# Kernel optimization log

Hardware: AMD Instinct MI355X
Metric: run time of the kernel (lower is better)

Reference implementation:

```python
import jax, jax.numpy as jnp
import numpy as np

DIM = 1024
N_HEADS = 16
HEAD_DIM = DIM // N_HEADS


def setup_inputs() -> dict:
    key = jax.random.key(0)
    k_x, k_wqkv, k_bqkv, k_wp, k_bp = jax.random.split(key, 5)
    s = 1.0 / np.sqrt(DIM)
    return {
        "x": jax.random.normal(k_x, (2, 2048, DIM), dtype=jnp.float32),
        "w_qkv": jax.random.uniform(k_wqkv, (3 * DIM, DIM), minval=-s, maxval=s, dtype=jnp.float32),
        "b_qkv": jax.random.uniform(k_bqkv, (3 * DIM,), minval=-s, maxval=s, dtype=jnp.float32),
        "w_proj": jax.random.uniform(k_wp, (DIM, DIM), minval=-s, maxval=s, dtype=jnp.float32),
        "b_proj": jax.random.uniform(k_bp, (DIM,), minval=-s, maxval=s, dtype=jnp.float32),
    }


def reference(x, w_qkv, b_qkv, w_proj, b_proj):
    B, S, D = x.shape
    H, Hd = N_HEADS, HEAD_DIM
    scale = jnp.asarray(Hd, x.dtype) ** 0.5
    qkv = x @ w_qkv.T + b_qkv                      # [B, S, 3D]
    q, k, v = jnp.split(qkv, 3, axis=-1)
    # [B, S, D] -> [B, H, S, Hd]
    q = q.reshape(B, S, H, Hd).transpose(0, 2, 1, 3)
    k = k.reshape(B, S, H, Hd).transpose(0, 2, 1, 3)
    v = v.reshape(B, S, H, Hd).transpose(0, 2, 1, 3)
    attn = jnp.einsum("bhqd,bhkd->bhqk", q, k) / scale
    attn = jax.nn.softmax(attn, axis=-1)
    out = jnp.einsum("bhqk,bhkd->bhqd", attn, v)   # [B, H, S, Hd]
    out = out.transpose(0, 2, 1, 3).reshape(B, S, D)
    return out @ w_proj.T + b_proj
```

## Files before the change

kernel.cpp:

```cpp
#include <hip/hip_runtime.h>

typedef __bf16 bf16;
typedef __bf16 bf16x4 __attribute__((ext_vector_type(4)));
typedef __bf16 bf16x8 __attribute__((ext_vector_type(8)));
typedef float f32x4 __attribute__((ext_vector_type(4)));
typedef float f32x16 __attribute__((ext_vector_type(16)));

#define DIMD 1024
#define NHEAD 16
#define HDIM 64
#define BATCH 2
#define SEQ 2048
#define MTOT (BATCH*SEQ)

#define EXP2F(x) __builtin_amdgcn_exp2f(x)

#define OFF_XB (0ull)
#define OFF_OB (0ull)
#define OFF_VT (8ull<<20)
#define OFF_WP (8ull<<20)

__device__ __forceinline__ void g2l16(const void* g, void* l) {
  __builtin_amdgcn_global_load_lds(
      (const __attribute__((address_space(1))) void*)g,
      (__attribute__((address_space(3))) void*)l,
      16, 0, 0);
}

__device__ __forceinline__ bf16x8 cvt8(float4 a, float4 b) {
  bf16x8 r = { (bf16)a.x, (bf16)a.y, (bf16)a.z, (bf16)a.w,
               (bf16)b.x, (bf16)b.y, (bf16)b.z, (bf16)b.w };
  return r;
}

__global__ __launch_bounds__(256) void cvt_kernel(const float* __restrict__ in,
                                                  bf16* __restrict__ out, int n4) {
  int i = blockIdx.x * blockDim.x + threadIdx.x;
  if (i < n4) {
    float4 v = ((const float4*)in)[i];
    bf16x4 o = { (bf16)v.x, (bf16)v.y, (bf16)v.z, (bf16)v.w };
    ((bf16x4*)out)[i] = o;
  }
}

__global__ __launch_bounds__(256, 3) void gemm_qkv(
    const bf16* __restrict__ A, const float* __restrict__ W,
    const float* __restrict__ bias,
    bf16* __restrict__ Qb, bf16* __restrict__ Kb, bf16* __restrict__ Vt)
{
  __shared__ bf16 lA[2][128 * 32];
  __shared__ bf16 lB[2][128 * 32];
  const int tid = threadIdx.x;
  const int wave = tid >> 6, lane = tid & 63;
  const int l15 = lane & 15, quad = lane >> 4;
  const int wm = wave >> 1, wn = wave & 1;
  const int tm = blockIdx.y * 128, tn = blockIdx.x * 128;

  f32x4 acc[4][4] = {};

  const int srow = tid >> 2, sch = (tid & 3) * 8;
  const bf16*  ga = &A[(size_t)(tm + srow) * DIMD + sch];
  const float* gb = &W[(size_t)(tn + srow) * DIMD + sch];

  g2l16(ga,                     &lA[0][wave * 512]);
  g2l16(ga + (size_t)64 * DIMD, &lA[0][2048 + wave * 512]);
  float4 bv0 = ((const float4*)gb)[0], bv1 = ((const float4*)gb)[1];
  float4 bv2 = ((const float4*)(gb + (size_t)64 * DIMD))[0],
         bv3 = ((const float4*)(gb + (size_t)64 * DIMD))[1];

  for (int kt = 0; kt < 32; kt++) {
    bf16* sB = lB[kt & 1];
    *(bf16x8*)&sB[srow * 32 + sch]        = cvt8(bv0, bv1);
    *(bf16x8*)&sB[(64 + srow) * 32 + sch] = cvt8(bv2, bv3);
    __syncthreads();

    if (kt < 31) {
      const int kn = (kt + 1) * 32;
      bf16* nA = lA[(kt + 1) & 1];
      g2l16(ga + kn,                     &nA[wave * 512]);
      g2l16(ga + kn + (size_t)64 * DIMD, &nA[2048 + wave * 512]);
      const float* gbn = gb + kn;
      bv0 = ((const float4*)gbn)[0]; bv1 = ((const float4*)gbn)[1];
      bv2 = ((const float4*)(gbn + (size_t)64 * DIMD))[0];
      bv3 = ((const float4*)(gbn + (size_t)64 * DIMD))[1];
    }

    const bf16* sA = lA[kt & 1];
    bf16x8 af[4], bfr[4];
#pragma unroll
    for (int i = 0; i < 4; i++)
      af[i] = *(const bf16x8*)&sA[(wm * 64 + i * 16 + l15) * 32 + quad * 8];
#pragma unroll
    for (int i = 0; i < 4; i++)
      bfr[i] = *(const bf16x8*)&sB[(wn * 64 + i * 16 + l15) * 32 + quad * 8];
#pragma unroll
    for (int i = 0; i < 4; i++)
#pragma unroll
      for (int j = 0; j < 4; j++)
        acc[i][j] = __builtin_amdgcn_mfma_f32_16x16x32_bf16(af[i], bfr[j], acc[i][j], 0, 0, 0);
  }

  const int sel = tn >> 10;
#pragma unroll
  for (int j = 0; j < 4; j++) {
    const int n = tn + wn * 64 + j * 16 + l15;
    const float bv = bias[n];
    const int d = n & 1023, h = d >> 6, hd = d & 63;
#pragma unroll
    for (int i = 0; i < 4; i++) {
      const int mbase = tm + wm * 64 + i * 16 + quad * 4;
      const int b = mbase >> 11, s0 = mbase & 2047;
      const int bh = b * NHEAD + h;
      if (sel == 2) {
        bf16x4 vv = { (bf16)(acc[i][j][0] + bv), (bf16)(acc[i][j][1] + bv),
                      (bf16)(acc[i][j][2] + bv), (bf16)(acc[i][j][3] + bv) };
        *(bf16x4*)&Vt[((size_t)bh * HDIM + hd) * SEQ + s0] = vv;
      } else {
#pragma unroll
        for (int r = 0; r < 4; r++) {
          float v = acc[i][j][r] + bv;
          if (sel == 0)
            Qb[((size_t)bh * SEQ + s0 + r) * HDIM + hd] = (bf16)(v * 0.18033688f);
          else
            Kb[((size_t)bh * SEQ + s0 + r) * HDIM + hd] = (bf16)v;
        }
      }
    }
  }
}

__global__ __launch_bounds__(256, 2) void gemm_proj(
    const bf16* __restrict__ A, const bf16* __restrict__ Bt,
    const float* __restrict__ bias, float* __restrict__ out)
{
  __shared__ bf16 lA[2][64 * 32];
  __shared__ bf16 lB[2][128 * 32];
  const int tid = threadIdx.x;
  const int wave = tid >> 6, lane = tid & 63;
  const int l15 = lane & 15, quad = lane >> 4;
  const int tm = blockIdx.y * 64, tn = blockIdx.x * 128;

  f32x4 acc[4][2] = {};

  const int srow = tid >> 2, sch = (tid & 3) * 8;
  const bf16* ga = &A[(size_t)(tm + srow) * DIMD + sch];
  const bf16* gb = &Bt[(size_t)(tn + srow) * DIMD + sch];

  g2l16(ga,                     &lA[0][wave * 512]);
  g2l16(gb,                     &lB[0][wave * 512]);
  g2l16(gb + (size_t)64 * DIMD, &lB[0][2048 + wave * 512]);

  for (int kt = 0; kt < 32; kt++) {
    __syncthreads();

    if (kt < 31) {
      const int kn = (kt + 1) * 32;
      bf16* nA = lA[(kt + 1) & 1];
      bf16* nB = lB[(kt + 1) & 1];
      g2l16(ga + kn,                     &nA[wave * 512]);
      g2l16(gb + kn,                     &nB[wave * 512]);
      g2l16(gb + kn + (size_t)64 * DIMD, &nB[2048 + wave * 512]);
    }

    const bf16* sA = lA[kt & 1];
    const bf16* sB = lB[kt & 1];
    bf16x8 af[4], bfr[2];
#pragma unroll
    for (int i = 0; i < 4; i++)
      af[i] = *(const bf16x8*)&sA[(i * 16 + l15) * 32 + quad * 8];
#pragma unroll
    for (int j = 0; j < 2; j++)
      bfr[j] = *(const bf16x8*)&sB[(wave * 32 + j * 16 + l15) * 32 + quad * 8];
#pragma unroll
    for (int i = 0; i < 4; i++)
#pragma unroll
      for (int j = 0; j < 2; j++)
        acc[i][j] = __builtin_amdgcn_mfma_f32_16x16x32_bf16(af[i], bfr[j], acc[i][j], 0, 0, 0);
  }

#pragma unroll
  for (int j = 0; j < 2; j++) {
    const int n = tn + wave * 32 + j * 16 + l15;
    const float bv = bias[n];
#pragma unroll
    for (int i = 0; i < 4; i++) {
      const int mbase = tm + i * 16 + quad * 4;
#pragma unroll
      for (int r = 0; r < 4; r++)
        out[(size_t)(mbase + r) * DIMD + n] = acc[i][j][r] + bv;
    }
  }
}

__global__ __launch_bounds__(256, 2) void attn_kernel(
    const bf16* __restrict__ Qb, const bf16* __restrict__ Kb,
    const bf16* __restrict__ Vt, bf16* __restrict__ Ob)
{
  __shared__ bf16 lK[2][64 * 64];
  __shared__ bf16 lP[4][32 * 64];

  const int tid = threadIdx.x;
  const int wave = tid >> 6, lane = tid & 63;
  const int l31 = lane & 31, h = lane >> 5;
  const int xcd = blockIdx.x & 7, grp = blockIdx.x >> 3;
  const int bh = xcd + 8 * (grp & 3);
  const int qt = grp >> 2;

  const int qrow = qt * 128 + wave * 32 + l31;
  const bf16* qp = Qb + ((size_t)bh * SEQ + qrow) * HDIM + h * 8;
  bf16x8 qf[4];
#pragma unroll
  for (int c = 0; c < 4; c++) qf[c] = *(const bf16x8*)(qp + c * 16);

  const int srow = tid >> 3;
  const int sch = (tid & 7) * 8;
  const bf16* kg = Kb + ((size_t)bh * SEQ + srow) * HDIM + sch;
  uint4 kr0 = *(const uint4*)(kg);
  uint4 kr1 = *(const uint4*)(kg + 32 * HDIM);
  const int swb = (sch * 2) ^ ((srow & 7) << 4);

  const bf16* vg0 = Vt + ((size_t)bh * HDIM + l31) * SEQ + h * 8;
  const bf16* vg1 = vg0 + (size_t)32 * SEQ;
  bf16x8 vf0[4], vf1[4];

  char* pw = (char*)lP[wave];
  const int px = (l31 & 7) << 4;

  f32x16 o0 = {}, o1 = {};
  float mrow = -1e30f, lrow = 0.f;

  for (int kt = 0; kt < SEQ / 64; kt++) {
    char* sK = (char*)lK[kt & 1];
    *(uint4*)(sK + srow * 128 + swb)        = kr0;
    *(uint4*)(sK + (32 + srow) * 128 + swb) = kr1;
    __syncthreads();

    const int ktn = (kt + 1) & (SEQ / 64 - 1);
    kr0 = *(const uint4*)(kg + (size_t)ktn * 64 * HDIM);
    kr1 = *(const uint4*)(kg + (size_t)ktn * 64 * HDIM + 32 * HDIM);

    f32x16 s0 = {}, s1 = {};
    __builtin_amdgcn_s_setprio(1);
#pragma unroll
    for (int c = 0; c < 4; c++) {
      bf16x8 k0 = *(const bf16x8*)(sK + l31 * 128 + (((c * 32) + h * 16) ^ px));
      bf16x8 k1 = *(const bf16x8*)(sK + (32 + l31) * 128 + (((c * 32) + h * 16) ^ px));
      s0 = __builtin_amdgcn_mfma_f32_32x32x16_bf16(k0, qf[c], s0, 0, 0, 0);
      s1 = __builtin_amdgcn_mfma_f32_32x32x16_bf16(k1, qf[c], s1, 0, 0, 0);
    }

    if (kt > 0) {
#pragma unroll
      for (int c = 0; c < 4; c++) {
        bf16x8 pf = *(const bf16x8*)(pw + l31 * 128 + (((c * 32) + h * 16) ^ px));
        o0 = __builtin_amdgcn_mfma_f32_32x32x16_bf16(vf0[c], pf, o0, 0, 0, 0);
        o1 = __builtin_amdgcn_mfma_f32_32x32x16_bf16(vf1[c], pf, o1, 0, 0, 0);
      }
    }
    __builtin_amdgcn_s_setprio(0);

#pragma unroll
    for (int c = 0; c < 4; c++) {
      vf0[c] = *(const bf16x8*)(vg0 + (size_t)kt * 64 + c * 16);
      vf1[c] = *(const bf16x8*)(vg1 + (size_t)kt * 64 + c * 16);
    }

    float a[16];
#pragma unroll
    for (int r = 0; r < 8; r++)
      a[r] = fmaxf(fmaxf(s0[r], s0[r + 8]), fmaxf(s1[r], s1[r + 8]));
#pragma unroll
    for (int r = 0; r < 4; r++) a[r] = fmaxf(a[r], a[r + 4]);
    float mx = fmaxf(fmaxf(a[0], a[1]), fmaxf(a[2], a[3]));
    mx = fmaxf(mx, __shfl_xor(mx, 32, 64));

    if (!__all(mx - mrow <= 8.0f)) {
      const float nm = fmaxf(mrow, mx);
      const float alpha = EXP2F(mrow - nm);
      mrow = nm;
      lrow *= alpha;
#pragma unroll
      for (int r = 0; r < 16; r++) { o0[r] *= alpha; o1[r] *= alpha; }
    }

#pragma unroll
    for (int r = 0; r < 16; r++) {
      const float p0 = EXP2F(s0[r] - mrow);
      const float p1 = EXP2F(s1[r] - mrow);
      s0[r] = p0; s1[r] = p1;
      a[r] = p0 + p1;
    }
#pragma unroll
    for (int r = 0; r < 8; r++) a[r] += a[r + 8];
#pragma unroll
    for (int r = 0; r < 4; r++) a[r] += a[r + 4];
    float rs = (a[0] + a[1]) + (a[2] + a[3]);
    rs += __shfl_xor(rs, 32, 64);
    lrow += rs;

#pragma unroll
    for (int g = 0; g < 4; g++) {
      bf16x4 pa = { (bf16)s0[4*g], (bf16)s0[4*g+1], (bf16)s0[4*g+2], (bf16)s0[4*g+3] };
      bf16x4 pb = { (bf16)s1[4*g], (bf16)s1[4*g+1], (bf16)s1[4*g+2], (bf16)s1[4*g+3] };
      *(bf16x4*)(pw + l31 * 128 + (((g * 16) + h * 8) ^ px))      = pa;
      *(bf16x4*)(pw + l31 * 128 + ((64 + (g * 16) + h * 8) ^ px)) = pb;
    }
  }

#pragma unroll
  for (int c = 0; c < 4; c++) {
    bf16x8 pf = *(const bf16x8*)(pw + l31 * 128 + (((c * 32) + h * 16) ^ px));
    o0 = __builtin_amdgcn_mfma_f32_32x32x16_bf16(vf0[c], pf, o0, 0, 0, 0);
    o1 = __builtin_amdgcn_mfma_f32_32x32x16_bf16(vf1[c], pf, o1, 0, 0, 0);
  }

  const int b = bh >> 4, head = bh & 15;
  const float inv = 1.f / lrow;
  const size_t base = ((size_t)b * SEQ + qrow) * DIMD + head * HDIM;
#pragma unroll
  for (int g = 0; g < 4; g++) {
    bf16x4 oa = { (bf16)(o0[4*g] * inv), (bf16)(o0[4*g+1] * inv),
                  (bf16)(o0[4*g+2] * inv), (bf16)(o0[4*g+3] * inv) };
    bf16x4 ob = { (bf16)(o1[4*g] * inv), (bf16)(o1[4*g+1] * inv),
                  (bf16)(o1[4*g+2] * inv), (bf16)(o1[4*g+3] * inv) };
    *(bf16x4*)&Ob[base + g * 8 + h * 4]      = oa;
    *(bf16x4*)&Ob[base + 32 + g * 8 + h * 4] = ob;
  }
}

extern "C" void kernel_launch(void* const* d_in, const int* in_sizes, int n_in,
                              void* d_out, int out_size, void* d_ws, size_t ws_size,
                              hipStream_t stream) {
  const float* x      = (const float*)d_in[0];
  const float* w_qkv  = (const float*)d_in[1];
  const float* b_qkv  = (const float*)d_in[2];
  const float* w_proj = (const float*)d_in[3];
  const float* b_proj = (const float*)d_in[4];
  float* out = (float*)d_out;
  char* ws = (char*)d_ws;

  bf16* Qb = (bf16*)d_out;
  bf16* Kb = (bf16*)d_out + (size_t)MTOT * DIMD;
  bf16* xb     = (bf16*)(ws + OFF_XB);
  bf16* Ob     = (bf16*)(ws + OFF_OB);
  bf16* Vt     = (bf16*)(ws + OFF_VT);
  bf16* wprojb = (bf16*)(ws + OFF_WP);

  cvt_kernel<<<(MTOT * DIMD / 4) / 256, 256, 0, stream>>>(x, xb, MTOT * DIMD / 4);
  gemm_qkv<<<dim3(24, 32), 256, 0, stream>>>(xb, w_qkv, b_qkv, Qb, Kb, Vt);
  attn_kernel<<<BATCH * NHEAD * (SEQ / 128), 256, 0, stream>>>(Qb, Kb, Vt, Ob);
  cvt_kernel<<<(DIMD * DIMD / 4) / 256, 256, 0, stream>>>(w_proj, wprojb, DIMD * DIMD / 4);
  gemm_proj<<<dim3(8, 64), 256, 0, stream>>>(Ob, wprojb, b_proj, out);
}
```

Before: 209.0 us.

## Restructure attention loop with 128-key tiles, shared V in LDS, register P shuffle

Widens the key tile from 64 to 128 and stages both K and V tiles in padded LDS, shared by all waves, instead of each wave loading V fragments from global memory. P is passed to the PV MFMA through cross-half lane shuffles in registers rather than a per-wave LDS round trip. The software pipeline that overlapped the previous tile's PV with the current QK^T is removed, and the conditional lazy rescale is replaced by an unconditional rescale every tile. This trades redundant global V traffic and P LDS writes for an extra barrier per tile and less overlap between the QK and PV stages.

```diff
diff --git a/kernel.cpp b/kernel.cpp
--- a/kernel.cpp
+++ b/kernel.cpp
@@ -192,12 +192,15 @@
   }
 }
 
+#define KTILE 128
+#define KSTR 72
+#define VSTR 136
 __global__ __launch_bounds__(256, 2) void attn_kernel(
     const bf16* __restrict__ Qb, const bf16* __restrict__ Kb,
     const bf16* __restrict__ Vt, bf16* __restrict__ Ob)
 {
-  __shared__ bf16 lK[2][64 * 64];
-  __shared__ bf16 lP[4][32 * 64];
+  __shared__ bf16 lK[KTILE * KSTR];
+  __shared__ bf16 lV[64 * VSTR];
 
   const int tid = threadIdx.x;
   const int wave = tid >> 6, lane = tid & 63;
@@ -215,103 +218,134 @@
   const int srow = tid >> 3;
   const int sch = (tid & 7) * 8;
   const bf16* kg = Kb + ((size_t)bh * SEQ + srow) * HDIM + sch;
-  uint4 kr0 = *(const uint4*)(kg);
-  uint4 kr1 = *(const uint4*)(kg + 32 * HDIM);
-  const int swb = (sch * 2) ^ ((srow & 7) << 4);
-
-  const bf16* vg0 = Vt + ((size_t)bh * HDIM + l31) * SEQ + h * 8;
-  const bf16* vg1 = vg0 + (size_t)32 * SEQ;
-  bf16x8 vf0[4], vf1[4];
-
-  char* pw = (char*)lP[wave];
-  const int px = (l31 & 7) << 4;
+  const bf16* vg = Vt + ((size_t)bh * HDIM + srow) * SEQ + sch;
+
+  uint4 kr[4], vr[4];
+#pragma unroll
+  for (int i = 0; i < 4; i++)
+    kr[i] = *(const uint4*)(kg + (size_t)(32 * i) * HDIM);
+#pragma unroll
+  for (int i = 0; i < 2; i++)
+#pragma unroll
+    for (int j = 0; j < 2; j++)
+      vr[i * 2 + j] = *(const uint4*)(vg + (size_t)(32 * i) * SEQ + j * 64);
+
+#pragma unroll
+  for (int i = 0; i < 4; i++)
+    *(uint4*)&lK[(srow + 32 * i) * KSTR + sch] = kr[i];
+#pragma unroll
+  for (int i = 0; i < 2; i++)
+#pragma unroll
+    for (int j = 0; j < 2; j++)
+      *(uint4*)&lV[(srow + 32 * i) * VSTR + j * 64 + sch] = vr[i * 2 + j];
 
   f32x16 o0 = {}, o1 = {};
   float mrow = -1e30f, lrow = 0.f;
 
-  for (int kt = 0; kt < SEQ / 64; kt++) {
-    char* sK = (char*)lK[kt & 1];
-    *(uint4*)(sK + srow * 128 + swb)        = kr0;
-    *(uint4*)(sK + (32 + srow) * 128 + swb) = kr1;
+  for (int kt = 0; kt < SEQ / KTILE; kt++) {
     __syncthreads();
 
-    const int ktn = (kt + 1) & (SEQ / 64 - 1);
-    kr0 = *(const uint4*)(kg + (size_t)ktn * 64 * HDIM);
-    kr1 = *(const uint4*)(kg + (size_t)ktn * 64 * HDIM + 32 * HDIM);
-
-    f32x16 s0 = {}, s1 = {};
-    __builtin_amdgcn_s_setprio(1);
+    if (kt < SEQ / KTILE - 1) {
+      const size_t koff = (size_t)(kt + 1) * KTILE;
+#pragma unroll
+      for (int i = 0; i < 4; i++)
+        kr[i] = *(const uint4*)(kg + (koff + 32 * i) * HDIM);
+#pragma unroll
+      for (int i = 0; i < 2; i++)
+#pragma unroll
+        for (int j = 0; j < 2; j++)
+          vr[i * 2 + j] = *(const uint4*)(vg + (size_t)(32 * i) * SEQ + koff + j * 64);
+    }
+
+    f32x16 s0 = {}, s1 = {}, s2 = {}, s3 = {};
 #pragma unroll
     for (int c = 0; c < 4; c++) {
-      bf16x8 k0 = *(const bf16x8*)(sK + l31 * 128 + (((c * 32) + h * 16) ^ px));
-      bf16x8 k1 = *(const bf16x8*)(sK + (32 + l31) * 128 + (((c * 32) + h * 16) ^ px));
+      bf16x8 k0 = *(const bf16x8*)&lK[(l31)       * KSTR + c * 16 + h * 8];
+      bf16x8 k1 = *(const bf16x8*)&lK[(32 + l31)  * KSTR + c * 16 + h * 8];
+      bf16x8 k2 = *(const bf16x8*)&lK[(64 + l31)  * KSTR + c * 16 + h * 8];
+      bf16x8 k3 = *(const bf16x8*)&lK[(96 + l31)  * KSTR + c * 16 + h * 8];
       s0 = __builtin_amdgcn_mfma_f32_32x32x16_bf16(k0, qf[c], s0, 0, 0, 0);
       s1 = __builtin_amdgcn_mfma_f32_32x32x16_bf16(k1, qf[c], s1, 0, 0, 0);
-    }
-
-    if (kt > 0) {
-#pragma unroll
-      for (int c = 0; c < 4; c++) {
-        bf16x8 pf = *(const bf16x8*)(pw + l31 * 128 + (((c * 32) + h * 16) ^ px));
-        o0 = __builtin_amdgcn_mfma_f32_32x32x16_bf16(vf0[c], pf, o0, 0, 0, 0);
-        o1 = __builtin_amdgcn_mfma_f32_32x32x16_bf16(vf1[c], pf, o1, 0, 0, 0);
-      }
-    }
-    __builtin_amdgcn_s_setprio(0);
-
-#pragma unroll
-    for (int c = 0; c < 4; c++) {
-      vf0[c] = *(const bf16x8*)(vg0 + (size_t)kt * 64 + c * 16);
-      vf1[c] = *(const bf16x8*)(vg1 + (size_t)kt * 64 + c * 16);
+      s2 = __builtin_amdgcn_mfma_f32_32x32x16_bf16(k2, qf[c], s2, 0, 0, 0);
+      s3 = __builtin_amdgcn_mfma_f32_32x32x16_bf16(k3, qf[c], s3, 0, 0, 0);
     }
 
     float a[16];
 #pragma unroll
-    for (int r = 0; r < 8; r++)
-      a[r] = fmaxf(fmaxf(s0[r], s0[r + 8]), fmaxf(s1[r], s1[r + 8]));
+    for (int r = 0; r < 16; r++)
+      a[r] = fmaxf(fmaxf(s0[r], s1[r]), fmaxf(s2[r], s3[r]));
+#pragma unroll
+    for (int r = 0; r < 8; r++) a[r] = fmaxf(a[r], a[r + 8]);
 #pragma unroll
     for (int r = 0; r < 4; r++) a[r] = fmaxf(a[r], a[r + 4]);
     float mx = fmaxf(fmaxf(a[0], a[1]), fmaxf(a[2], a[3]));
     mx = fmaxf(mx, __shfl_xor(mx, 32, 64));
 
-    if (!__all(mx - mrow <= 8.0f)) {
-      const float nm = fmaxf(mrow, mx);
-      const float alpha = EXP2F(mrow - nm);
-      mrow = nm;
-      lrow *= alpha;
-#pragma unroll
-      for (int r = 0; r < 16; r++) { o0[r] *= alpha; o1[r] *= alpha; }
-    }
+    const float nm = fmaxf(mrow, mx);
+    const float alpha = EXP2F(mrow - nm);
+    mrow = nm;
 
 #pragma unroll
     for (int r = 0; r < 16; r++) {
-      const float p0 = EXP2F(s0[r] - mrow);
-      const float p1 = EXP2F(s1[r] - mrow);
-      s0[r] = p0; s1[r] = p1;
-      a[r] = p0 + p1;
-    }
+      s0[r] = EXP2F(s0[r] - nm);
+      s1[r] = EXP2F(s1[r] - nm);
+      s2[r] = EXP2F(s2[r] - nm);
+      s3[r] = EXP2F(s3[r] - nm);
+    }
+#pragma unroll
+    for (int r = 0; r < 16; r++)
+      a[r] = (s0[r] + s1[r]) + (s2[r] + s3[r]);
 #pragma unroll
     for (int r = 0; r < 8; r++) a[r] += a[r + 8];
 #pragma unroll
     for (int r = 0; r < 4; r++) a[r] += a[r + 4];
     float rs = (a[0] + a[1]) + (a[2] + a[3]);
     rs += __shfl_xor(rs, 32, 64);
-    lrow += rs;
+    lrow = lrow * alpha + rs;
+
+#pragma unroll
+    for (int r = 0; r < 16; r++) { o0[r] *= alpha; o1[r] *= alpha; }
 
 #pragma unroll
     for (int g = 0; g < 4; g++) {
-      bf16x4 pa = { (bf16)s0[4*g], (bf16)s0[4*g+1], (bf16)s0[4*g+2], (bf16)s0[4*g+3] };
-      bf16x4 pb = { (bf16)s1[4*g], (bf16)s1[4*g+1], (bf16)s1[4*g+2], (bf16)s1[4*g+3] };
-      *(bf16x4*)(pw + l31 * 128 + (((g * 16) + h * 8) ^ px))      = pa;
-      *(bf16x4*)(pw + l31 * 128 + ((64 + (g * 16) + h * 8) ^ px)) = pb;
-    }
-  }
-
-#pragma unroll
-  for (int c = 0; c < 4; c++) {
-    bf16x8 pf = *(const bf16x8*)(pw + l31 * 128 + (((c * 32) + h * 16) ^ px));
-    o0 = __builtin_amdgcn_mfma_f32_32x32x16_bf16(vf0[c], pf, o0, 0, 0, 0);
-    o1 = __builtin_amdgcn_mfma_f32_32x32x16_bf16(vf1[c], pf, o1, 0, 0, 0);
+      const f32x16& sg = (g == 0) ? s0 : (g == 1) ? s1 : (g == 2) ? s2 : s3;
+#pragma unroll
+      for (int cp = 0; cp < 2; cp++) {
+        bf16x4 pk0 = { (bf16)sg[8 * cp + 0], (bf16)sg[8 * cp + 1],
+                       (bf16)sg[8 * cp + 2], (bf16)sg[8 * cp + 3] };
+        bf16x4 pk1 = { (bf16)sg[8 * cp + 4], (bf16)sg[8 * cp + 5],
+                       (bf16)sg[8 * cp + 6], (bf16)sg[8 * cp + 7] };
+        uint2 w0 = *(uint2*)&pk0;
+        uint2 w1 = *(uint2*)&pk1;
+        unsigned send0 = h ? w0.x : w1.x;
+        unsigned send1 = h ? w0.y : w1.y;
+        unsigned recv0 = __shfl_xor(send0, 32, 64);
+        unsigned recv1 = __shfl_xor(send1, 32, 64);
+        union { unsigned u[4]; bf16x8 v; } f;
+        f.u[0] = h ? recv0 : w0.x;
+        f.u[1] = h ? recv1 : w0.y;
+        f.u[2] = h ? w1.x : recv0;
+        f.u[3] = h ? w1.y : recv1;
+        const int cc = 2 * g + cp;
+        bf16x8 v0 = *(const bf16x8*)&lV[(l31)      * VSTR + cc * 16 + h * 8];
+        bf16x8 v1 = *(const bf16x8*)&lV[(32 + l31) * VSTR + cc * 16 + h * 8];
+        o0 = __builtin_amdgcn_mfma_f32_32x32x16_bf16(v0, f.v, o0, 0, 0, 0);
+        o1 = __builtin_amdgcn_mfma_f32_32x32x16_bf16(v1, f.v, o1, 0, 0, 0);
+      }
+    }
+
+    __syncthreads();
+
+    if (kt < SEQ / KTILE - 1) {
+#pragma unroll
+      for (int i = 0; i < 4; i++)
+        *(uint4*)&lK[(srow + 32 * i) * KSTR + sch] = kr[i];
+#pragma unroll
+      for (int i = 0; i < 2; i++)
+#pragma unroll
+        for (int j = 0; j < 2; j++)
+          *(uint4*)&lV[(srow + 32 * i) * VSTR + j * 64 + sch] = vr[i * 2 + j];
+    }
   }
 
   const int b = bh >> 4, head = bh & 15;
```

Result: slower. 231.7 us (+10.9%).
